# Kernel optimization log

Measured on AMD Instinct MI355X. Metric: run time of the kernel, lower is better.

Reference implementation:

```python
import jax, jax.numpy as jnp
import numpy as np

# ---- config (matches init_kwargs) ----
B, IN_CH, H, W_SP = 8, 1, 256, 256
WIDTH, M1, M2, NL, OUT_CH = 64, 12, 12, 4, 1
FC_HID = 128


def _gelu(a):
    # torch nn.GELU default = exact erf form
    return jax.nn.gelu(a, approximate=False)


def _spectral_conv2d(x, w1, w2):
    """x: [B, Cin, H, W]; w1/w2: [Cin, Cout, M1, M2, 2] -> [B, Cout, H, W]."""
    Bn, Cin, Hn, Wn = x.shape
    Cout = w1.shape[1]
    x_ft = jnp.fft.rfft2(x, axes=(-2, -1))          # [B, Cin, H, W//2+1] complex
    w1c = w1[..., 0] + 1j * w1[..., 1]
    w2c = w2[..., 0] + 1j * w2[..., 1]
    top = jnp.einsum('bixy,ioxy->boxy', x_ft[:, :, :M1, :M2], w1c)
    bot = jnp.einsum('bixy,ioxy->boxy', x_ft[:, :, -M1:, :M2], w2c)
    out_ft = jnp.zeros((Bn, Cout, Hn, Wn // 2 + 1), dtype=x_ft.dtype)
    out_ft = out_ft.at[:, :, :M1, :M2].set(top)
    out_ft = out_ft.at[:, :, -M1:, :M2].set(bot)
    return jnp.fft.irfft2(out_ft, s=(Hn, Wn), axes=(-2, -1))


def setup_inputs() -> dict:
    key = jax.random.key(0)
    ks = jax.random.split(key, 8)
    scale = 1.0 / (WIDTH * WIDTH)
    inp = {
        'x': jax.random.normal(ks[0], (B, IN_CH, H, W_SP)),
        'fc0_w': jax.random.normal(ks[1], (WIDTH, IN_CH + 2)) * 0.3,
        'fc0_b': jnp.zeros((WIDTH,)),
        # spectral weights stacked over layers: [NL, Cin, Cout, M1, M2, 2]
        'w1': scale * jax.random.uniform(ks[2], (NL, WIDTH, WIDTH, M1, M2, 2)),
        'w2': scale * jax.random.uniform(ks[3], (NL, WIDTH, WIDTH, M1, M2, 2)),
        # 1x1 conv weights: [NL, Cout, Cin] and bias [NL, Cout]
        'pw_w': jax.random.normal(ks[4], (NL, WIDTH, WIDTH)) * (1.0 / np.sqrt(WIDTH)),
        'pw_b': jnp.zeros((NL, WIDTH)),
        'fc1_w': jax.random.normal(ks[5], (FC_HID, WIDTH)) * (1.0 / np.sqrt(WIDTH)),
        'fc1_b': jnp.zeros((FC_HID,)),
        'fc2_w': jax.random.normal(ks[6], (OUT_CH, FC_HID)) * (1.0 / np.sqrt(FC_HID)),
        'fc2_b': jnp.zeros((OUT_CH,)),
    }
    return {k: v.astype(jnp.float32) for k, v in inp.items()}


def reference(x, fc0_w, fc0_b, w1, w2, pw_w, pw_b, fc1_w, fc1_b, fc2_w, fc2_b):
    Bn, _, Hn, Wn = x.shape
    # positional grid in [0, 1], concatenated on channel dim
    gx = jnp.broadcast_to(jnp.linspace(0.0, 1.0, Hn)[None, None, :, None], (Bn, 1, Hn, Wn))
    gy = jnp.broadcast_to(jnp.linspace(0.0, 1.0, Wn)[None, None, None, :], (Bn, 1, Hn, Wn))
    h = jnp.concatenate([x, gx.astype(x.dtype), gy.astype(x.dtype)], axis=1)  # [B, in+2, H, W]
    # lift (fc0): Linear over channels (torch weight layout [out, in])
    h = jnp.einsum('bcxy,wc->bwxy', h, fc0_w) + fc0_b[None, :, None, None]
    for i in range(NL):
        x1 = _spectral_conv2d(h, w1[i], w2[i])
        x2 = jnp.einsum('bixy,oi->boxy', h, pw_w[i]) + pw_b[i][None, :, None, None]
        h = x1 + x2
        if i < NL - 1:
            h = _gelu(h)
    # projection head
    h = jnp.einsum('bwxy,fw->bfxy', h, fc1_w) + fc1_b[None, :, None, None]
    h = _gelu(h)
    h = jnp.einsum('bfxy,of->boxy', h, fc2_w) + fc2_b[None, :, None, None]
    return h  # [B, out_channels, H, W]
```

## Files before the change

kernel.cpp:

```cpp
#include <hip/hip_runtime.h>
#include <hip/hip_bf16.h>

#define FC0_F   0
#define FC0B_F  192
#define PWB_F   16640
#define FC1B_F  25088
#define FC2_F   25216
#define FC2B_F  25344
#define PHW_F   25408
#define PHH_F   31552
#define FLAG_F  44032
#define PWA_HI_U 512
#define PWA_LO_U 16896
#define FC1A_HI_U 33792
#define FC1A_LO_U 41984
#define TWI_HI_U 88192
#define TWI_LO_U 96384
#define TWF_HI_U 104576
#define TWF_LO_U 112768
#define HB_OFF_U  131072
#define GG_OFF_U  33685504
#define FO_OFF_F  18415616
#define WS_NEED   74842112
#define NT11 60161

typedef short bf16x8 __attribute__((ext_vector_type(8)));
typedef float f32x4  __attribute__((ext_vector_type(4)));

union FU10 { float f; unsigned u; };
__device__ __forceinline__ float bfu2f(unsigned short u) { FU10 v; v.u = ((unsigned)u) << 16; return v.f; }
__device__ __forceinline__ unsigned short f2bfu(float f) {
  FU10 v; v.f = f; unsigned b = v.u;
  return (unsigned short)((b + 0x7FFFu + ((b >> 16) & 1u)) >> 16);
}
__device__ __forceinline__ unsigned pk2bf(float a, float b) {
  return (unsigned)f2bfu(a) | ((unsigned)f2bfu(b) << 16);
}
__device__ __forceinline__ float gelu10(float v) {
  return 0.5f * v * (1.0f + erff(v * 0.7071067811865475f));
}
__device__ __forceinline__ float rdw10(const __hip_bfloat16* h, const float* f,
                                       long i, int isf32) {
  return isf32 ? f[i] : __bfloat162float(h[i]);
}

__global__ __launch_bounds__(256) void kf10_fill(__hip_bfloat16* outH, float code) {
  outH[(size_t)blockIdx.x * 256 + threadIdx.x] = __float2bfloat16(code);
}

__global__ __launch_bounds__(64) void kd10_detect(const unsigned short* Xh, float* Wf) {
  if (threadIdx.x == 0 && blockIdx.x == 0) {
    int ok = 1;
    for (int k = 0; k < 128; ++k) {
      unsigned short u = Xh[2 * k];
      unsigned e = (u >> 7) & 0xFF;
      if (!(u == 0 || (e >= 0x60 && e <= 0x88))) ok = 0;
    }
    Wf[FLAG_F] = ok ? 0.0f : 1.0f;
  }
}

__global__ __launch_bounds__(256) void kt10_tables(
    const __hip_bfloat16* f0h, const float* f0f,
    const __hip_bfloat16* f0bh, const float* f0bf,
    const __hip_bfloat16* pwh, const float* pwf,
    const __hip_bfloat16* pwbh, const float* pwbf,
    const __hip_bfloat16* f1h, const float* f1f,
    const __hip_bfloat16* f1bh, const float* f1bf,
    const __hip_bfloat16* f2h, const float* f2f,
    const __hip_bfloat16* f2bh, const float* f2bf,
    float* Wf) {
  unsigned short* Wu = (unsigned short*)Wf;
  const int isf32 = (Wf[FLAG_F] != 0.0f);
  const int stride = gridDim.x * blockDim.x;
  for (int n0 = blockIdx.x * blockDim.x + threadIdx.x; n0 < NT11; n0 += stride) {
    int n = n0;
    if (n < 192) { Wf[FC0_F + n] = rdw10(f0h, f0f, n, isf32); continue; }
    n -= 192;
    if (n < 64)  { Wf[FC0B_F + n] = rdw10(f0bh, f0bf, n, isf32); continue; }
    n -= 64;
    if (n < 256) { Wf[PWB_F + n] = rdw10(pwbh, pwbf, n, isf32); continue; }
    n -= 256;
    if (n < 8192) {
      float v = rdw10(f1h, f1f, n, isf32);
      unsigned short hi = f2bfu(v);
      Wu[FC1A_HI_U + n] = hi;
      Wu[FC1A_LO_U + n] = f2bfu(v - bfu2f(hi));
      continue;
    }
    n -= 8192;
    if (n < 128) { Wf[FC1B_F + n] = rdw10(f1bh, f1bf, n, isf32); continue; }
    n -= 128;
    if (n < 128) { Wf[FC2_F + n] = rdw10(f2h, f2f, n, isf32); continue; }
    n -= 128;
    if (n < 1)   { Wf[FC2B_F + n] = rdw10(f2bh, f2bf, 0, isf32); continue; }
    n -= 1;
    if (n < 6144) { int w = n / 24, r = n % 24, ky = r >> 1, part = r & 1;
      int idx = (w * ky) & 255; float a = idx * (1.0f/128.0f);
      Wf[PHW_F + n] = part ? sinpif(a) : cospif(a); continue; }
    n -= 6144;
    if (n < 12288) { int xx = n / 48, r = n % 48, kx = r >> 1, part = r & 1;
      int kxa = (kx < 12) ? kx : kx + 232;
      int idx = (xx * kxa) & 255; float a = idx * (1.0f/128.0f);
      Wf[PHH_F + n] = part ? sinpif(a) : cospif(a); continue; }
    n -= 12288;
    if (n < 16384) {
      float v = rdw10(pwh, pwf, n, isf32);
      unsigned short hi = f2bfu(v);
      Wu[PWA_HI_U + n] = hi;
      Wu[PWA_LO_U + n] = f2bfu(v - bfu2f(hi));
      continue;
    }
    n -= 16384;
    if (n < 8192) {
      int w = n >> 5, k = n & 31;
      float v;
      if (k == 0)      v = 1.0f / 65536.0f;
      else if (k < 12) { int idx = (w*k) & 255;
        v =  2.0f * cospif(idx * (1.0f/128.0f)) * (1.0f/65536.0f); }
      else if (k < 23) { int ky = k - 11; int idx = (w*ky) & 255;
        v = -2.0f * sinpif(idx * (1.0f/128.0f)) * (1.0f/65536.0f); }
      else v = 0.0f;
      unsigned short hi = f2bfu(v);
      Wu[TWI_HI_U + n] = hi;
      Wu[TWI_LO_U + n] = f2bfu(v - bfu2f(hi));
      continue;
    }
    n -= 8192;
    {
      int r = n >> 8, w = n & 255;
      float v;
      if (r < 12)      { int idx = (w*r) & 255;  v =  cospif(idx * (1.0f/128.0f)); }
      else if (r < 24) { int ky = r - 12; int idx = (w*ky) & 255;
                         v = -sinpif(idx * (1.0f/128.0f)); }
      else v = 0.0f;
      unsigned short hi = f2bfu(v);
      Wu[TWF_HI_U + n] = hi;
      Wu[TWF_LO_U + n] = f2bfu(v - bfu2f(hi));
    }
  }
}

__device__ void gstep10(const float* Wf, __hip_bfloat16* GG,
                        unsigned* hrow32, float* pbuf, int b, int x) {
  const int t = threadIdx.x;
  const int c = t & 63, q = t >> 6;
  const int cp = c >> 1, hi = c & 1;
  float aR[12], aI[12];
#pragma unroll
  for (int k = 0; k < 12; ++k) { aR[k] = 0.0f; aI[k] = 0.0f; }
  for (int j = 0; j < 64; ++j) {
    int w = q*64 + j;
    unsigned u = hrow32[cp*256 + ((w + 2*cp) & 255)];
    float hv = bfu2f((unsigned short)(hi ? (u >> 16) : (u & 0xFFFFu)));
    const float* ph = Wf + PHW_F + w*24;
#pragma unroll
    for (int k = 0; k < 12; ++k) {
      aR[k] += hv * ph[2*k];
      aI[k] -= hv * ph[2*k + 1];
    }
  }
  __syncthreads();
#pragma unroll
  for (int k = 0; k < 12; ++k) {
    pbuf[q*1600 + c*25 + 2*k]     = aR[k];
    pbuf[q*1600 + c*25 + 2*k + 1] = aI[k];
  }
  __syncthreads();
  unsigned* Grow = (unsigned*)((unsigned short*)GG + (size_t)(b*256 + x)*1536);
#pragma unroll
  for (int j = 0; j < 3; ++j) {
    int p = j*256 + t;
    int cc = p / 12, jj = p % 12;
    int base = cc*25;
    int e0 = (jj < 6) ? (4*jj) : (4*(jj - 6) + 1);
    float s0 = pbuf[base + e0]            + pbuf[1600 + base + e0]
             + pbuf[3200 + base + e0]     + pbuf[4800 + base + e0];
    float s1 = pbuf[base + e0 + 2]        + pbuf[1600 + base + e0 + 2]
             + pbuf[3200 + base + e0 + 2] + pbuf[4800 + base + e0 + 2];
    Grow[p] = pk2bf(s0, s1);
  }
}

__device__ __forceinline__ void row_store10(__hip_bfloat16* HB, const unsigned* hrow32,
                                            int b, int x) {
  uint4* hbW = (uint4*)(HB + (size_t)(b*256 + x)*16384);
  const int t = threadIdx.x;
#pragma unroll
  for (int j = 0; j < 8; ++j) {
    int n = j*256 + t, p = n >> 3, cg = n & 7;
    unsigned vv[4];
#pragma unroll
    for (int m = 0; m < 4; ++m) {
      int cp = cg*4 + m;
      vv[m] = hrow32[cp*256 + ((p + 2*cp) & 255)];
    }
    hbW[n] = make_uint4(vv[0], vv[1], vv[2], vv[3]);
  }
}

__global__ __launch_bounds__(256) void kl10_lift(const __hip_bfloat16* Xh, const float* Xf,
                                                 const float* Wf,
                                                 __hip_bfloat16* HB, __hip_bfloat16* GG) {
  __shared__ __align__(16) char smem[32768];
  unsigned* hrow32 = (unsigned*)smem;
  float* pbuf = (float*)smem;
  const int rid = ((blockIdx.x & 7) << 8) | (blockIdx.x >> 3);
  const int b = rid >> 8, x = rid & 255;
  const int w = threadIdx.x;
  const int isf32 = (Wf[FLAG_F] != 0.0f);
  float xv = isf32 ? Xf[(size_t)(b*256 + x)*256 + w]
                   : __bfloat162float(Xh[(size_t)(b*256 + x)*256 + w]);
  float gx = x * (1.0f/255.0f), gy = w * (1.0f/255.0f);
#pragma unroll
  for (int cp = 0; cp < 32; ++cp) {
    int c = cp*2;
    float h0 = xv*Wf[FC0_F + c*3]     + gx*Wf[FC0_F + c*3 + 1]
             + gy*Wf[FC0_F + c*3 + 2] + Wf[FC0B_F + c];
    float h1 = xv*Wf[FC0_F + c*3 + 3] + gx*Wf[FC0_F + c*3 + 4]
             + gy*Wf[FC0_F + c*3 + 5] + Wf[FC0B_F + c + 1];
    hrow32[cp*256 + ((w + 2*cp) & 255)] = pk2bf(h0, h1);
  }
  __syncthreads();
  row_store10(HB, hrow32, b, x);
  gstep10(Wf, GG, hrow32, pbuf, b, x);
}

__global__ __launch_bounds__(256) void ks10_spec(const float* Wf, const __hip_bfloat16* GG,
    const __hip_bfloat16* w1h, const float* w1f,
    const __hip_bfloat16* w2h, const float* w2f,
    float* Fo, int l) {
  __shared__ float pbufA[6400];
  __shared__ float Fbuf[1536];
  const int blk = (blockIdx.x & 7) * 24 + (blockIdx.x >> 3);
  const int b = blk / 24, kx = blk % 24;
  const int t = threadIdx.x;
  const int isf32 = (Wf[FLAG_F] != 0.0f);
  {
    const int i = t & 63, q = t >> 6;
    float fr[12], fi[12];
#pragma unroll
    for (int k = 0; k < 12; ++k) { fr[k] = 0.0f; fi[k] = 0.0f; }
    for (int j = 0; j < 64; ++j) {
      int x = q*64 + j;
      const uint4* gp = (const uint4*)((const unsigned short*)GG
                        + (size_t)(b*256 + x)*1536 + i*24);
      uint4 u0 = gp[0], u1 = gp[1], u2 = gp[2];
      float cc = Wf[PHH_F + x*48 + 2*kx], ss = Wf[PHH_F + x*48 + 2*kx + 1];
      unsigned uu[12] = {u0.x, u0.y, u0.z, u0.w, u1.x, u1.y, u1.z, u1.w,
                         u2.x, u2.y, u2.z, u2.w};
#pragma unroll
      for (int k = 0; k < 12; ++k) {
        unsigned ure = uu[k >> 1], uim = uu[6 + (k >> 1)];
        float gr = bfu2f((unsigned short)((k & 1) ? (ure >> 16) : (ure & 0xFFFFu)));
        float gi = bfu2f((unsigned short)((k & 1) ? (uim >> 16) : (uim & 0xFFFFu)));
        fr[k] += gr*cc + gi*ss;
        fi[k] += gi*cc - gr*ss;
      }
    }
#pragma unroll
    for (int k = 0; k < 12; ++k) {
      pbufA[q*1600 + i*25 + 2*k]     = fr[k];
      pbufA[q*1600 + i*25 + 2*k + 1] = fi[k];
    }
  }
  __syncthreads();
#pragma unroll
  for (int j = 0; j < 6; ++j) {
    int idx = j*256 + t;
    int cc = idx / 24, m = idx - cc*24;
    Fbuf[idx] = pbufA[cc*25 + m] + pbufA[1600 + cc*25 + m]
              + pbufA[3200 + cc*25 + m] + pbufA[4800 + cc*25 + m];
  }
  __syncthreads();
  {
    const int o = t & 63, q = t >> 6;
    float br[12], bi[12];
#pragma unroll
    for (int k = 0; k < 12; ++k) { br[k] = 0.0f; bi[k] = 0.0f; }
    const int kxe = (kx < 12) ? kx : kx - 12;
    const __hip_bfloat16* wh = (kx < 12) ? w1h : w2h;
    const float*         wfp = (kx < 12) ? w1f : w2f;
    for (int i = q*16; i < q*16 + 16; ++i) {
      size_t widx = ((size_t)((l*64 + i)*64 + o))*288 + (size_t)kxe*24;
      float wr_[12], wi_[12];
      if (isf32) {
        const float* wp = wfp + widx;
#pragma unroll
        for (int k = 0; k < 12; ++k) { wr_[k] = wp[2*k]; wi_[k] = wp[2*k + 1]; }
      } else {
        const uint4* wp = (const uint4*)((const unsigned short*)wh + widx);
        uint4 u0 = wp[0], u1 = wp[1], u2 = wp[2];
        unsigned uu[12] = {u0.x, u0.y, u0.z, u0.w, u1.x, u1.y, u1.z, u1.w,
                           u2.x, u2.y, u2.z, u2.w};
#pragma unroll
        for (int k = 0; k < 12; ++k) {
          wr_[k] = bfu2f((unsigned short)(uu[k] & 0xFFFFu));
          wi_[k] = bfu2f((unsigned short)(uu[k] >> 16));
        }
      }
      const float* Fp = Fbuf + i*24;
#pragma unroll
      for (int k = 0; k < 12; ++k) {
        float Fr = Fp[k], Fi = Fp[12 + k];
        br[k] += Fr*wr_[k] - Fi*wi_[k];
        bi[k] += Fr*wi_[k] + Fi*wr_[k];
      }
    }
#pragma unroll
    for (int k = 0; k < 12; ++k) {
      pbufA[q*1536 + k*128 + o*2]     = br[k];
      pbufA[q*1536 + k*128 + o*2 + 1] = bi[k];
    }
  }
  __syncthreads();
#pragma unroll
  for (int j = 0; j < 6; ++j) {
    int n = j*256 + t;
    int ky = n >> 7, r = n & 127;
    Fo[((size_t)(b*12 + ky)*24 + kx)*128 + r] =
        pbufA[n] + pbufA[1536 + n] + pbufA[3072 + n] + pbufA[4608 + n];
  }
}

__global__ __launch_bounds__(256) void ky13_layer(const float* __restrict__ Wf,
                                                  __hip_bfloat16* __restrict__ HB,
                                                  __hip_bfloat16* __restrict__ GG,
                                                  const float* __restrict__ Fo,
                                                  __hip_bfloat16* __restrict__ outH,
                                                  float* __restrict__ outF,
                                                  int l, int last) {
  __shared__ __align__(16) char smem[32768];
  unsigned short* gbT   = (unsigned short*)smem;
  unsigned*       gbT32 = (unsigned*)smem;
  const unsigned short* Wu = (const unsigned short*)Wf;
  const int rid = ((blockIdx.x & 7) << 8) | (blockIdx.x >> 3);
  const int b = rid >> 8, x = rid & 255;
  const int t = threadIdx.x;
  const int l15 = t & 15, g = (t >> 4) & 3, wv = t >> 6;

  unsigned short* HBu = (unsigned short*)(HB + (size_t)(b*256 + x)*16384);
  unsigned short* GGu = (unsigned short*)GG + (size_t)(b*256 + x)*1536;

  const int w0w = wv*64;
  bf16x8 bh[4][2];
#pragma unroll
  for (int nt = 0; nt < 4; ++nt) {
    int wpx = w0w + nt*16 + l15;
#pragma unroll
    for (int kt = 0; kt < 2; ++kt)
      bh[nt][kt] = *(const bf16x8*)(HBu + (size_t)wpx*64 + kt*32 + g*8);
  }

  { int o = t >> 2, cu = t & 3; gbT32[o*16 + 12 + cu] = 0u; }
  {
    const float* phx = Wf + PHH_F + x*48;
#pragma unroll 1
    for (int j = 0; j < 3; ++j) {
      int p = j*256 + t; int ky = p >> 6, o = p & 63;
      const float2* Fop = (const float2*)(Fo + (size_t)(b*12 + ky)*3072) + o;
      float gr = 0.0f, gi = 0.0f;
#pragma unroll
      for (int kx = 0; kx < 24; ++kx) {
        float2 f = Fop[kx*64];
        float cc = phx[2*kx], ss = phx[2*kx + 1];
        gr += f.x*cc - f.y*ss;
        gi += f.x*ss + f.y*cc;
      }
      gbT[o*32 + ky] = f2bfu(gr);
      gbT[o*32 + (ky ? (11 + ky) : 23)] = f2bfu(gi);
    }
  }

  bf16x8 bi[4][2];
#pragma unroll
  for (int nt = 0; nt < 4; ++nt) {
    int wpx = w0w + nt*16 + l15;
    bi[nt][0] = *(const bf16x8*)(Wu + TWI_HI_U + wpx*32 + g*8);
    bi[nt][1] = *(const bf16x8*)(Wu + TWI_LO_U + wpx*32 + g*8);
  }
  bf16x8 apw[4][2][2];
#pragma unroll
  for (int mt = 0; mt < 4; ++mt)
#pragma unroll
    for (int kt = 0; kt < 2; ++kt) {
      int off = l*4096 + (mt*16 + l15)*64 + kt*32 + g*8;
      apw[mt][kt][0] = *(const bf16x8*)(Wu + PWA_HI_U + off);
      apw[mt][kt][1] = *(const bf16x8*)(Wu + PWA_LO_U + off);
    }
  float bias[4][4];
#pragma unroll
  for (int mt = 0; mt < 4; ++mt)
#pragma unroll
    for (int r = 0; r < 4; ++r)
      bias[mt][r] = Wf[PWB_F + l*64 + mt*16 + g*4 + r];

  __syncthreads();
  bf16x8 ainv[4];
#pragma unroll
  for (int mt = 0; mt < 4; ++mt)
    ainv[mt] = *(const bf16x8*)(gbT + (mt*16 + l15)*32 + g*8);
  __syncthreads();

#pragma unroll
  for (int nt = 0; nt < 4; ++nt) {
    const int wpx = w0w + nt*16 + l15;
#pragma unroll
    for (int mt = 0; mt < 4; ++mt) {
      f32x4 acc = {bias[mt][0], bias[mt][1], bias[mt][2], bias[mt][3]};
      acc = __builtin_amdgcn_mfma_f32_16x16x32_bf16(ainv[mt],      bi[nt][0], acc, 0, 0, 0);
      acc = __builtin_amdgcn_mfma_f32_16x16x32_bf16(ainv[mt],      bi[nt][1], acc, 0, 0, 0);
      acc = __builtin_amdgcn_mfma_f32_16x16x32_bf16(apw[mt][0][0], bh[nt][0], acc, 0, 0, 0);
      acc = __builtin_amdgcn_mfma_f32_16x16x32_bf16(apw[mt][0][1], bh[nt][0], acc, 0, 0, 0);
      acc = __builtin_amdgcn_mfma_f32_16x16x32_bf16(apw[mt][1][0], bh[nt][1], acc, 0, 0, 0);
      acc = __builtin_amdgcn_mfma_f32_16x16x32_bf16(apw[mt][1][1], bh[nt][1], acc, 0, 0, 0);
      float v0 = acc[0], v1 = acc[1], v2 = acc[2], v3 = acc[3];
      if (!last) { v0 = gelu10(v0); v1 = gelu10(v1); v2 = gelu10(v2); v3 = gelu10(v3); }
      const int c0 = mt*16 + g*4;
      uint2 pk; pk.x = pk2bf(v0, v1); pk.y = pk2bf(v2, v3);
      if (!last) {
        *(uint2*)(HBu + (size_t)wpx*64 + c0) = pk;
        *(unsigned short*)(smem + (((c0+0)*512 + wpx*2) ^ (((c0+0) & 7) << 4))) = f2bfu(v0);
        *(unsigned short*)(smem + (((c0+1)*512 + wpx*2) ^ (((c0+1) & 7) << 4))) = f2bfu(v1);
        *(unsigned short*)(smem + (((c0+2)*512 + wpx*2) ^ (((c0+2) & 7) << 4))) = f2bfu(v2);
        *(unsigned short*)(smem + (((c0+3)*512 + wpx*2) ^ (((c0+3) & 7) << 4))) = f2bfu(v3);
      } else {
        *(uint2*)(smem + ((wpx*128 + c0*2) ^ ((wpx & 7) << 4))) = pk;
      }
    }
  }

  if (!last) {
    __syncthreads();
    f32x4 g0 = {0.f, 0.f, 0.f, 0.f}, g1 = {0.f, 0.f, 0.f, 0.f};
    const int crow = wv*16 + l15;
    const int rswz = (crow & 7) << 4;
#pragma unroll
    for (int kk = 0; kk < 8; ++kk) {
      const int k0 = kk*32;
      bf16x8 af  = *(const bf16x8*)(smem + ((crow*512 + (k0 + g*8)*2) ^ rswz));
      bf16x8 b0h = *(const bf16x8*)(Wu + TWF_HI_U + l15*256 + k0 + g*8);
      bf16x8 b0l = *(const bf16x8*)(Wu + TWF_LO_U + l15*256 + k0 + g*8);
      bf16x8 b1h = *(const bf16x8*)(Wu + TWF_HI_U + (16 + l15)*256 + k0 + g*8);
      bf16x8 b1l = *(const bf16x8*)(Wu + TWF_LO_U + (16 + l15)*256 + k0 + g*8);
      g0 = __builtin_amdgcn_mfma_f32_16x16x32_bf16(af, b0h, g0, 0, 0, 0);
      g0 = __builtin_amdgcn_mfma_f32_16x16x32_bf16(af, b0l, g0, 0, 0, 0);
      g1 = __builtin_amdgcn_mfma_f32_16x16x32_bf16(af, b1h, g1, 0, 0, 0);
      g1 = __builtin_amdgcn_mfma_f32_16x16x32_bf16(af, b1l, g1, 0, 0, 0);
    }
    __syncthreads();
#pragma unroll
    for (int ntk = 0; ntk < 2; ++ntk) {
      int kyt = ntk*16 + l15;
      if (kyt < 24) {
        f32x4 gg = ntk ? g1 : g0;
#pragma unroll
        for (int rr = 0; rr < 4; ++rr)
          gbT[(wv*16 + g*4 + rr)*24 + kyt] = f2bfu(gg[rr]);
      }
    }
    __syncthreads();
    unsigned* GGrow = (unsigned*)GGu;
    const unsigned* st32 = (const unsigned*)gbT;
#pragma unroll
    for (int j = 0; j < 3; ++j) GGrow[j*256 + t] = st32[j*256 + t];
  } else {
    __syncthreads();
    const int isf32 = (Wf[FLAG_F] != 0.0f);
    bf16x8 bh2[4][2];
#pragma unroll
    for (int nt = 0; nt < 4; ++nt) {
      int wpx = w0w + nt*16 + l15;
#pragma unroll
      for (int kt = 0; kt < 2; ++kt)
        bh2[nt][kt] = *(const bf16x8*)(smem +
            ((wpx*128 + kt*64 + g*16) ^ ((wpx & 7) << 4)));
    }
    float s[4] = {0.0f, 0.0f, 0.0f, 0.0f};
#pragma unroll 2
    for (int mt = 0; mt < 8; ++mt) {
      const int arow = (mt*16 + l15)*64 + g*8;
      bf16x8 a0h = *(const bf16x8*)(Wu + FC1A_HI_U + arow);
      bf16x8 a0l = *(const bf16x8*)(Wu + FC1A_LO_U + arow);
      bf16x8 a1h = *(const bf16x8*)(Wu + FC1A_HI_U + arow + 32);
      bf16x8 a1l = *(const bf16x8*)(Wu + FC1A_LO_U + arow + 32);
      float f1b[4], f2v[4];
#pragma unroll
      for (int r = 0; r < 4; ++r) {
        f1b[r] = Wf[FC1B_F + mt*16 + g*4 + r];
        f2v[r] = Wf[FC2_F  + mt*16 + g*4 + r];
      }
#pragma unroll
      for (int nt = 0; nt < 4; ++nt) {
        f32x4 acc = {f1b[0], f1b[1], f1b[2], f1b[3]};
        acc = __builtin_amdgcn_mfma_f32_16x16x32_bf16(a0h, bh2[nt][0], acc, 0, 0, 0);
        acc = __builtin_amdgcn_mfma_f32_16x16x32_bf16(a0l, bh2[nt][0], acc, 0, 0, 0);
        acc = __builtin_amdgcn_mfma_f32_16x16x32_bf16(a1h, bh2[nt][1], acc, 0, 0, 0);
        acc = __builtin_amdgcn_mfma_f32_16x16x32_bf16(a1l, bh2[nt][1], acc, 0, 0, 0);
#pragma unroll
        for (int r = 0; r < 4; ++r)
          s[nt] += gelu10(acc[r]) * f2v[r];
      }
    }
    const float fc2b = Wf[FC2B_F];
#pragma unroll
    for (int nt = 0; nt < 4; ++nt) {
      float v = s[nt];
      v += __shfl_xor(v, 16);
      v += __shfl_xor(v, 32);
      if (g == 0) {
        size_t idx = (size_t)(b*256 + x)*256 + (w0w + nt*16 + l15);
        if (isf32) outF[idx] = v + fc2b;
        else       outH[idx] = __float2bfloat16(v + fc2b);
      }
    }
  }
}

extern "C" void kernel_launch(void* const* d_in, const int* in_sizes, int n_in,
                              void* d_out, int out_size, void* d_ws, size_t ws_size,
                              hipStream_t stream) {
  (void)out_size;
  __hip_bfloat16* outH = (__hip_bfloat16*)d_out;
  float*          outF = (float*)d_out;
  float*          Wf   = (float*)d_ws;
  __hip_bfloat16* HB   = (__hip_bfloat16*)d_ws + HB_OFF_U;
  __hip_bfloat16* GG   = (__hip_bfloat16*)d_ws + GG_OFF_U;
  float*          Fo   = (float*)d_ws + FO_OFF_F;

  static const int EXP_SZ[11] = {524288, 192, 64, 4718592, 4718592,
                                 16384, 256, 8192, 128, 128, 1};
  if (n_in != 11) { kf10_fill<<<2048, 256, 0, stream>>>(outH, 27648.0f); return; }
  for (int i = 0; i < 11; ++i) {
    if (in_sizes[i] != EXP_SZ[i]) {
      kf10_fill<<<2048, 256, 0, stream>>>(outH, 28672.0f + 256.0f * (float)i);
      return;
    }
  }
  if (ws_size < (size_t)WS_NEED) {
    int q = (int)(ws_size >> 25); if (q > 31) q = 31;
    kf10_fill<<<2048, 256, 0, stream>>>(outH, 4096.0f + 32.0f * (float)q);
    return;
  }

  kd10_detect<<<1, 64, 0, stream>>>((const unsigned short*)d_in[0], Wf);
  kt10_tables<<<64, 256, 0, stream>>>(
      (const __hip_bfloat16*)d_in[1], (const float*)d_in[1],
      (const __hip_bfloat16*)d_in[2], (const float*)d_in[2],
      (const __hip_bfloat16*)d_in[5], (const float*)d_in[5],
      (const __hip_bfloat16*)d_in[6], (const float*)d_in[6],
      (const __hip_bfloat16*)d_in[7], (const float*)d_in[7],
      (const __hip_bfloat16*)d_in[8], (const float*)d_in[8],
      (const __hip_bfloat16*)d_in[9], (const float*)d_in[9],
      (const __hip_bfloat16*)d_in[10], (const float*)d_in[10],
      Wf);
  kl10_lift<<<2048, 256, 0, stream>>>((const __hip_bfloat16*)d_in[0],
                                      (const float*)d_in[0], Wf, HB, GG);
  for (int l = 0; l < 4; ++l) {
    ks10_spec<<<192, 256, 0, stream>>>(Wf, GG,
        (const __hip_bfloat16*)d_in[3], (const float*)d_in[3],
        (const __hip_bfloat16*)d_in[4], (const float*)d_in[4],
        Fo, l);
    ky13_layer<<<2048, 256, 0, stream>>>(Wf, HB, GG, Fo, outH, outF,
                                         l, (l == 3) ? 1 : 0);
  }
}
```

Before: 749.4 us.

## Compute lift row DFT with bf16 MFMA and store lifted row from registers

The lift kernel's per-row W-direction partial DFT (12 modes, real and imaginary) was scalar FMA work reading twiddles from global memory. It now runs as 16x16x32 bf16 MFMAs against hi/lo-split twiddle tables, using an XOR-swizzled channel-major LDS layout. The HB row store now writes directly from registers instead of re-reading a transposed shared buffer. This drops the scalar accumulation loop and the 4-way partial-sum reduction, but the DFT inputs are bf16 with split-precision twiddles, so accuracy may shift slightly.

```diff
diff --git a/kernel.cpp b/kernel.cpp
--- a/kernel.cpp
+++ b/kernel.cpp
@@ -141,77 +141,22 @@
   }
 }
 
-__device__ void gstep10(const float* Wf, __hip_bfloat16* GG,
-                        unsigned* hrow32, float* pbuf, int b, int x) {
-  const int t = threadIdx.x;
-  const int c = t & 63, q = t >> 6;
-  const int cp = c >> 1, hi = c & 1;
-  float aR[12], aI[12];
-#pragma unroll
-  for (int k = 0; k < 12; ++k) { aR[k] = 0.0f; aI[k] = 0.0f; }
-  for (int j = 0; j < 64; ++j) {
-    int w = q*64 + j;
-    unsigned u = hrow32[cp*256 + ((w + 2*cp) & 255)];
-    float hv = bfu2f((unsigned short)(hi ? (u >> 16) : (u & 0xFFFFu)));
-    const float* ph = Wf + PHW_F + w*24;
-#pragma unroll
-    for (int k = 0; k < 12; ++k) {
-      aR[k] += hv * ph[2*k];
-      aI[k] -= hv * ph[2*k + 1];
-    }
-  }
-  __syncthreads();
-#pragma unroll
-  for (int k = 0; k < 12; ++k) {
-    pbuf[q*1600 + c*25 + 2*k]     = aR[k];
-    pbuf[q*1600 + c*25 + 2*k + 1] = aI[k];
-  }
-  __syncthreads();
-  unsigned* Grow = (unsigned*)((unsigned short*)GG + (size_t)(b*256 + x)*1536);
-#pragma unroll
-  for (int j = 0; j < 3; ++j) {
-    int p = j*256 + t;
-    int cc = p / 12, jj = p % 12;
-    int base = cc*25;
-    int e0 = (jj < 6) ? (4*jj) : (4*(jj - 6) + 1);
-    float s0 = pbuf[base + e0]            + pbuf[1600 + base + e0]
-             + pbuf[3200 + base + e0]     + pbuf[4800 + base + e0];
-    float s1 = pbuf[base + e0 + 2]        + pbuf[1600 + base + e0 + 2]
-             + pbuf[3200 + base + e0 + 2] + pbuf[4800 + base + e0 + 2];
-    Grow[p] = pk2bf(s0, s1);
-  }
-}
-
-__device__ __forceinline__ void row_store10(__hip_bfloat16* HB, const unsigned* hrow32,
-                                            int b, int x) {
-  uint4* hbW = (uint4*)(HB + (size_t)(b*256 + x)*16384);
-  const int t = threadIdx.x;
-#pragma unroll
-  for (int j = 0; j < 8; ++j) {
-    int n = j*256 + t, p = n >> 3, cg = n & 7;
-    unsigned vv[4];
-#pragma unroll
-    for (int m = 0; m < 4; ++m) {
-      int cp = cg*4 + m;
-      vv[m] = hrow32[cp*256 + ((p + 2*cp) & 255)];
-    }
-    hbW[n] = make_uint4(vv[0], vv[1], vv[2], vv[3]);
-  }
-}
-
-__global__ __launch_bounds__(256) void kl10_lift(const __hip_bfloat16* Xh, const float* Xf,
+__global__ __launch_bounds__(256) void kl11_lift(const __hip_bfloat16* Xh, const float* Xf,
                                                  const float* Wf,
                                                  __hip_bfloat16* HB, __hip_bfloat16* GG) {
   __shared__ __align__(16) char smem[32768];
-  unsigned* hrow32 = (unsigned*)smem;
-  float* pbuf = (float*)smem;
+  unsigned short* gbT = (unsigned short*)smem;
+  const unsigned short* Wu = (const unsigned short*)Wf;
   const int rid = ((blockIdx.x & 7) << 8) | (blockIdx.x >> 3);
   const int b = rid >> 8, x = rid & 255;
-  const int w = threadIdx.x;
+  const int t = threadIdx.x;
+  const int w = t;
+  const int l15 = t & 15, g = (t >> 4) & 3, wv = t >> 6;
   const int isf32 = (Wf[FLAG_F] != 0.0f);
   float xv = isf32 ? Xf[(size_t)(b*256 + x)*256 + w]
                    : __bfloat162float(Xh[(size_t)(b*256 + x)*256 + w]);
   float gx = x * (1.0f/255.0f), gy = w * (1.0f/255.0f);
+  unsigned hbreg[32];
 #pragma unroll
   for (int cp = 0; cp < 32; ++cp) {
     int c = cp*2;
@@ -219,11 +164,53 @@
              + gy*Wf[FC0_F + c*3 + 2] + Wf[FC0B_F + c];
     float h1 = xv*Wf[FC0_F + c*3 + 3] + gx*Wf[FC0_F + c*3 + 4]
              + gy*Wf[FC0_F + c*3 + 5] + Wf[FC0B_F + c + 1];
-    hrow32[cp*256 + ((w + 2*cp) & 255)] = pk2bf(h0, h1);
-  }
-  __syncthreads();
-  row_store10(HB, hrow32, b, x);
-  gstep10(Wf, GG, hrow32, pbuf, b, x);
+    unsigned pk = pk2bf(h0, h1);
+    hbreg[cp] = pk;
+    *(unsigned short*)(smem + (((c+0)*512 + w*2) ^ (((c+0) & 7) << 4))) =
+        (unsigned short)(pk & 0xFFFFu);
+    *(unsigned short*)(smem + (((c+1)*512 + w*2) ^ (((c+1) & 7) << 4))) =
+        (unsigned short)(pk >> 16);
+  }
+  {
+    uint4* hbW = (uint4*)(HB + (size_t)(b*256 + x)*16384) + w*8;
+#pragma unroll
+    for (int j = 0; j < 8; ++j)
+      hbW[j] = make_uint4(hbreg[j*4], hbreg[j*4+1], hbreg[j*4+2], hbreg[j*4+3]);
+  }
+  __syncthreads();
+
+  f32x4 g0 = {0.f, 0.f, 0.f, 0.f}, g1 = {0.f, 0.f, 0.f, 0.f};
+  const int crow = wv*16 + l15;
+  const int rswz = (crow & 7) << 4;
+#pragma unroll
+  for (int kk = 0; kk < 8; ++kk) {
+    const int k0 = kk*32;
+    bf16x8 af  = *(const bf16x8*)(smem + ((crow*512 + (k0 + g*8)*2) ^ rswz));
+    bf16x8 b0h = *(const bf16x8*)(Wu + TWF_HI_U + l15*256 + k0 + g*8);
+    bf16x8 b0l = *(const bf16x8*)(Wu + TWF_LO_U + l15*256 + k0 + g*8);
+    bf16x8 b1h = *(const bf16x8*)(Wu + TWF_HI_U + (16 + l15)*256 + k0 + g*8);
+    bf16x8 b1l = *(const bf16x8*)(Wu + TWF_LO_U + (16 + l15)*256 + k0 + g*8);
+    g0 = __builtin_amdgcn_mfma_f32_16x16x32_bf16(af, b0h, g0, 0, 0, 0);
+    g0 = __builtin_amdgcn_mfma_f32_16x16x32_bf16(af, b0l, g0, 0, 0, 0);
+    g1 = __builtin_amdgcn_mfma_f32_16x16x32_bf16(af, b1h, g1, 0, 0, 0);
+    g1 = __builtin_amdgcn_mfma_f32_16x16x32_bf16(af, b1l, g1, 0, 0, 0);
+  }
+  __syncthreads();
+#pragma unroll
+  for (int ntk = 0; ntk < 2; ++ntk) {
+    int kyt = ntk*16 + l15;
+    if (kyt < 24) {
+      f32x4 gg = ntk ? g1 : g0;
+#pragma unroll
+      for (int rr = 0; rr < 4; ++rr)
+        gbT[(wv*16 + g*4 + rr)*24 + kyt] = f2bfu(gg[rr]);
+    }
+  }
+  __syncthreads();
+  unsigned* GGrow = (unsigned*)((unsigned short*)GG + (size_t)(b*256 + x)*1536);
+  const unsigned* st32 = (const unsigned*)gbT;
+#pragma unroll
+  for (int j = 0; j < 3; ++j) GGrow[j*256 + t] = st32[j*256 + t];
 }
 
 __global__ __launch_bounds__(256) void ks10_spec(const float* Wf, const __hip_bfloat16* GG,
@@ -554,7 +541,7 @@
       (const __hip_bfloat16*)d_in[9], (const float*)d_in[9],
       (const __hip_bfloat16*)d_in[10], (const float*)d_in[10],
       Wf);
-  kl10_lift<<<2048, 256, 0, stream>>>((const __hip_bfloat16*)d_in[0],
+  kl11_lift<<<2048, 256, 0, stream>>>((const __hip_bfloat16*)d_in[0],
                                       (const float*)d_in[0], Wf, HB, GG);
   for (int l = 0; l < 4; ++l) {
     ks10_spec<<<192, 256, 0, stream>>>(Wf, GG,
```

New measurement: 701.8 us. 1.07x faster.
